# Performance work log

Measured on AMD Instinct MI355X. Metric: run time of the kernel, lower is better.

The kernel has to match this reference:

```python
import jax, jax.numpy as jnp
import numpy as np

TESS = 16            # number of tessellation cells on [0,1]
ZERO_BOUNDARY = False
N_POINTS = 16777216  # 2**24
EPS = 1e-7


def make_basis(nC, zero_boundary):
    # Constraint matrix L: continuity of v(x)=a_c x + b_c at internal vertices x_k=k/nC
    rows = []
    for k in range(1, nC):
        xk = k / nC
        r = np.zeros(2 * nC)
        r[2 * (k - 1)] = xk
        r[2 * (k - 1) + 1] = 1.0
        r[2 * k] = -xk
        r[2 * k + 1] = -1.0
        rows.append(r)
    if zero_boundary:
        r = np.zeros(2 * nC); r[1] = 1.0; rows.append(r)          # v(0)=0
        r = np.zeros(2 * nC); r[-2] = 1.0; r[-1] = 1.0; rows.append(r)  # v(1)=0
    L = np.stack(rows)
    _, _, Vh = np.linalg.svd(L, full_matrices=True)
    rank = np.linalg.matrix_rank(L)
    return np.ascontiguousarray(Vh[rank:].T).astype(np.float32)  # [2nC, d]

B_NP = make_basis(TESS, ZERO_BOUNDARY)


def setup_inputs() -> dict:
    key = jax.random.key(0)
    k1, k2 = jax.random.split(key)
    x = jax.random.uniform(k1, (N_POINTS, 1), dtype=jnp.float32)
    theta = jax.random.normal(k2, (1, B_NP.shape[1]), dtype=jnp.float32)
    return {"x": x, "theta": theta}


def cpab_integrate(grid, a, b, nC):
    """Exact closed-form integration of dx/dt = a_c x + b_c over t in [0,1].
    grid: [N]; a,b: [nC]. Returns (phi(x), log dphi/dx). At most nC cell hops."""
    h = 1.0 / nC
    c0 = jnp.clip(jnp.floor(grid * nC), 0, nC - 1).astype(jnp.int32)
    carry0 = (grid, c0, jnp.ones_like(grid), jnp.zeros_like(grid),
              jnp.zeros(grid.shape, dtype=bool))

    def step(carry, _):
        xc, c, t, phase, done = carry
        ac = a[c]
        bc = b[c]
        v = ac * xc + bc
        going_right = v >= 0
        # edge cells extend to +/- inf: moving outward never exits
        edge_out = (going_right & (c == nC - 1)) | ((~going_right) & (c == 0))
        xb = jnp.where(going_right, (c + 1).astype(grid.dtype) * h,
                       c.astype(grid.dtype) * h)
        vb = ac * xb + bc
        a_zero = jnp.abs(ac) < 1e-12
        v_zero = jnp.abs(v) < 1e-15
        ac_safe = jnp.where(a_zero, 1.0, ac)
        v_safe = jnp.where(v_zero, 1.0, v)
        ratio = vb / v_safe
        thit_lin = (xb - xc) / v_safe
        thit_aff = jnp.log(jnp.maximum(ratio, 1e-30)) / ac_safe
        thit = jnp.where(a_zero, thit_lin, thit_aff)
        reachable = (~edge_out) & (~v_zero) & (ratio > 0)
        thit = jnp.where(reachable, thit, jnp.inf)
        exit_ = (thit <= t) & (~done)
        dt = jnp.where(done, 0.0, jnp.where(exit_, thit, t))
        psi = jnp.where(a_zero, xc + v * dt,
                        (xc + bc / ac_safe) * jnp.exp(ac * dt) - bc / ac_safe)
        x_new = jnp.where(done, xc, jnp.where(exit_, xb, psi))
        phase_new = phase + jnp.where(done, 0.0, ac * dt)
        c_new = jnp.where(exit_, jnp.clip(c + jnp.where(going_right, 1, -1), 0, nC - 1), c)
        t_new = t - dt
        done_new = done | (~exit_)
        return (x_new, c_new, t_new, phase_new, done_new), None

    (xf, _, _, phase, _), _ = jax.lax.scan(step, carry0, None, length=nC)
    return xf, phase


def reference(x, theta):
    B = jnp.asarray(B_NP)
    grid = jnp.clip(x[:, 0], EPS, 1.0 - EPS)          # [N]
    A = (theta @ B.T).reshape(TESS, 2)                # theta batch of 1 -> [nC,2]
    a, b = A[:, 0], A[:, 1]
    z, phase = cpab_integrate(grid, a, b, TESS)
    # log dz/dx = sum_c a_c * dt_c = phase (log(exp(phase)) simplified)
    return z[:, None], phase[:, None]
```

## Files before the change

kernel.cpp:

```cpp
#include <hip/hip_runtime.h>
#include <math.h>

#define NCELL 16
#define BLOCK 256
#define H16 0.0625f
#define SENT 1e30f

struct BMat { float v[32][17]; };
static BMat g_B;

static struct BInitializer {
  BInitializer() {
    double A[15][32];
    for (int r = 0; r < 15; ++r)
      for (int j = 0; j < 32; ++j) A[r][j] = 0.0;
    for (int k = 1; k <= 15; ++k) {
      double xk = (double)k / 16.0;
      A[k - 1][2 * (k - 1)]     =  xk;
      A[k - 1][2 * (k - 1) + 1] =  1.0;
      A[k - 1][2 * k]           = -xk;
      A[k - 1][2 * k + 1]       = -1.0;
    }
    double V[15][32], tau[15];
    for (int i = 0; i < 15; ++i) {
      double alpha = A[i][i];
      double xn2 = 0.0;
      for (int j = i + 1; j < 32; ++j) xn2 += A[i][j] * A[i][j];
      for (int j = 0; j < 32; ++j) V[i][j] = 0.0;
      V[i][i] = 1.0;
      if (xn2 == 0.0) { tau[i] = 0.0; continue; }
      double beta = -copysign(sqrt(alpha * alpha + xn2), alpha);
      tau[i] = (beta - alpha) / beta;
      double s = 1.0 / (alpha - beta);
      for (int j = i + 1; j < 32; ++j) V[i][j] = A[i][j] * s;
      A[i][i] = beta;
      for (int r = i + 1; r < 15; ++r) {
        double dot = 0.0;
        for (int j = i; j < 32; ++j) dot += A[r][j] * V[i][j];
        double t = tau[i] * dot;
        for (int j = i; j < 32; ++j) A[r][j] -= t * V[i][j];
      }
    }
    for (int q = 0; q < 17; ++q) {
      double u[32];
      for (int p = 0; p < 32; ++p) u[p] = 0.0;
      u[15 + q] = 1.0;
      for (int i = 14; i >= 0; --i) {
        double dot = 0.0;
        for (int p = i; p < 32; ++p) dot += u[p] * V[i][p];
        double t = tau[i] * dot;
        for (int p = i; p < 32; ++p) u[p] -= t * V[i][p];
      }
      for (int p = 0; p < 32; ++p) g_B.v[p][q] = (float)u[p];
    }
  }
} g_binit;

__global__ __launch_bounds__(BLOCK) void
cpab_kernel(const float4* __restrict__ x4, const float* __restrict__ theta,
            float4* __restrict__ zout, float4* __restrict__ pout, BMat B) {
  __shared__ float Ash[32];
  __shared__ float4 cellT[2][16];
  __shared__ float vbT[2][17];
  __shared__ float lvbT[2][17];
  __shared__ float prT[2][17];

  const int tid = threadIdx.x;

  if (tid < 32) {
    float acc = 0.0f;
#pragma unroll
    for (int q = 0; q < 17; ++q) acc += theta[q] * B.v[tid][q];
    Ash[tid] = acc;
  }
  __syncthreads();

  if (tid < 32) {
    int d = tid >> 4, c = tid & 15;
    int cs = d ? 15 - c : c;
    float a = Ash[2 * cs];
    float b = d ? -(Ash[2 * cs] + Ash[2 * cs + 1]) : Ash[2 * cs + 1];
    float as = (fabsf(a) < 1e-12f) ? 1.0f : a;
    float ia = 1.0f / as;
    cellT[d][c] = make_float4(a, b, ia, b * ia);
  }
  if (tid >= 32 && tid < 66) {
    int t2 = tid - 32;
    int d = (t2 >= 17) ? 1 : 0, k = d ? t2 - 17 : t2;
    int c = min(k, 15);
    int cs = d ? 15 - c : c;
    float a = Ash[2 * cs];
    float b = d ? -(Ash[2 * cs] + Ash[2 * cs + 1]) : Ash[2 * cs + 1];
    float v = fmaf(a, (float)k * H16, b);
    vbT[d][k] = v;
    lvbT[d][k] = __logf(v);
  }
  __syncthreads();

  if (tid < 32) {
    int d = tid >> 4, c = tid & 15;
    float a = cellT[d][c].x, ia = cellT[d][c].z;
    float va = vbT[d][c], vb = vbT[d][c + 1];
    float tau;
    if (va > 0.0f && vb > 0.0f)
      tau = (fabsf(a) < 1e-12f) ? H16 / va : (lvbT[d][c + 1] - lvbT[d][c]) * ia;
    else
      tau = 2.0f;
    tau = fminf(fmaxf(tau, 0.0f), 2.0f);
    prT[d][c + 1] = tau;
  }
  __syncthreads();
  if (tid < 2) {
    float s = 0.0f;
    prT[tid][0] = 0.0f;
    for (int c = 0; c < 16; ++c) { s += prT[tid][c + 1]; prT[tid][c + 1] = s; }
  }
  __syncthreads();

  float prF[16], prM[16];
#pragma unroll
  for (int k = 0; k < 16; ++k) { prF[k] = prT[0][k]; prM[k] = prT[1][k]; }

  const int gid = blockIdx.x * BLOCK + tid;
  const float4 xs = x4[gid];
  float xin[4] = {xs.x, xs.y, xs.z, xs.w};
  float zr[4], ph[4];

#pragma unroll
  for (int p = 0; p < 4; ++p) {
    float x = fminf(fmaxf(xin[p], 1e-7f), 1.0f - 1e-7f);
    int c0 = min((int)(x * 16.0f), 15);
    float4 cf = cellT[0][c0];
    float vraw = fmaf(cf.x, x, cf.y);
    bool mir = vraw < 0.0f;
    int cw = mir ? 15 - c0 : c0;
    float xw = mir ? 1.0f - x : x;
    float a2 = cf.x;
    float ia2 = cf.z;
    float v0 = mir ? -vraw : vraw;
    bool az = fabsf(a2) < 1e-12f;
    float lv0 = __logf(v0);

    const float* vb  = vbT[mir ? 1 : 0];
    const float* lvb = lvbT[mir ? 1 : 0];
    const float* pr  = prT[mir ? 1 : 0];

    float xb = (float)(cw + 1) * H16;
    float vbn = vb[cw + 1];
    float rv = __builtin_amdgcn_rcpf(fmaxf(v0, 1e-30f));
    float t0 = az ? (xb - xw) * rv : (lvb[cw + 1] - lv0) * ia2;
    if (v0 < 1e-15f || vbn <= 0.0f) t0 = SENT;

    float prc = pr[cw + 1];
    float Tstar = 1.0f - t0 + prc;
    int m = cw;
#pragma unroll
    for (int k = 1; k <= 15; ++k) {
      float prk = mir ? prM[k] : prF[k];
      if ((k > cw) && (prk <= Tstar)) ++m;
    }
    bool moved = (m != cw);
    float4 cmv = cellT[mir ? 1 : 0][m];
    float t_enter = moved ? t0 + (pr[m] - prc) : 0.0f;
    float t_rem = 1.0f - t_enter;
    float xe = moved ? (float)m * H16 : xw;
    float ve = moved ? vb[m] : v0;
    bool az3 = fabsf(cmv.x) < 1e-12f;
    float zw = az3 ? fmaf(ve, t_rem, xe)
                   : fmaf(xe + cmv.w, __expf(cmv.x * t_rem), -cmv.w);
    zr[p] = mir ? 1.0f - zw : zw;
    ph[p] = (moved ? lvb[m] - lv0 : 0.0f) + cmv.x * t_rem;
  }

  zout[gid] = make_float4(zr[0], zr[1], zr[2], zr[3]);
  pout[gid] = make_float4(ph[0], ph[1], ph[2], ph[3]);
}

extern "C" void kernel_launch(void* const* d_in, const int* in_sizes, int n_in,
                              void* d_out, int out_size, void* d_ws, size_t ws_size,
                              hipStream_t stream) {
  const float4* x4 = (const float4*)d_in[0];
  const float* theta = (const float*)d_in[1];
  float* out = (float*)d_out;
  const int npts = in_sizes[0];
  const int groups = npts / 4;
  const int grid = groups / BLOCK;
  cpab_kernel<<<grid, BLOCK, 0, stream>>>(
      x4, theta, (float4*)out, (float4*)(out + npts), g_B);
}
```

Before: 195.5 us.

## Pack per-vertex tables into one float4 LDS array and binary-search exit cell

Merges the separate cell, boundary-velocity, log-velocity and prefix-time shared tables into a single float4 table per direction. Each lookup then needs one wide LDS read instead of several scalar ones. The 15-step linear scan over per-thread prefix arrays becomes a 4-step binary search over the shared prefix sums, which drops the 32 per-thread registers. Per-point reciprocals are now computed with rcp instead of being read from the table, which adds a little ALU work and slightly changes precision.

```diff
diff --git a/kernel.cpp b/kernel.cpp
--- a/kernel.cpp
+++ b/kernel.cpp
@@ -1,7 +1,6 @@
 #include <hip/hip_runtime.h>
 #include <math.h>
 
-#define NCELL 16
 #define BLOCK 256
 #define H16 0.0625f
 #define SENT 1e30f
@@ -60,10 +59,7 @@
 cpab_kernel(const float4* __restrict__ x4, const float* __restrict__ theta,
             float4* __restrict__ zout, float4* __restrict__ pout, BMat B) {
   __shared__ float Ash[32];
-  __shared__ float4 cellT[2][16];
-  __shared__ float vbT[2][17];
-  __shared__ float lvbT[2][17];
-  __shared__ float prT[2][17];
+  __shared__ float4 G[2][17];
 
   const int tid = threadIdx.x;
 
@@ -75,51 +71,39 @@
   }
   __syncthreads();
 
-  if (tid < 32) {
-    int d = tid >> 4, c = tid & 15;
-    int cs = d ? 15 - c : c;
-    float a = Ash[2 * cs];
-    float b = d ? -(Ash[2 * cs] + Ash[2 * cs + 1]) : Ash[2 * cs + 1];
-    float as = (fabsf(a) < 1e-12f) ? 1.0f : a;
-    float ia = 1.0f / as;
-    cellT[d][c] = make_float4(a, b, ia, b * ia);
-  }
-  if (tid >= 32 && tid < 66) {
-    int t2 = tid - 32;
-    int d = (t2 >= 17) ? 1 : 0, k = d ? t2 - 17 : t2;
-    int c = min(k, 15);
-    int cs = d ? 15 - c : c;
+  if (tid < 34) {
+    int d = (tid >= 17) ? 1 : 0, k = d ? tid - 17 : tid;
+    int c = min(k, 15), cs = d ? 15 - c : c;
     float a = Ash[2 * cs];
     float b = d ? -(Ash[2 * cs] + Ash[2 * cs + 1]) : Ash[2 * cs + 1];
     float v = fmaf(a, (float)k * H16, b);
-    vbT[d][k] = v;
-    lvbT[d][k] = __logf(v);
+    G[d][k].x = v;
+    G[d][k].y = __logf(v);
+    G[d][k].w = a;
   }
   __syncthreads();
 
   if (tid < 32) {
     int d = tid >> 4, c = tid & 15;
-    float a = cellT[d][c].x, ia = cellT[d][c].z;
-    float va = vbT[d][c], vb = vbT[d][c + 1];
+    float a = G[d][c].w;
+    float va = G[d][c].x, vb = G[d][c + 1].x;
     float tau;
-    if (va > 0.0f && vb > 0.0f)
-      tau = (fabsf(a) < 1e-12f) ? H16 / va : (lvbT[d][c + 1] - lvbT[d][c]) * ia;
-    else
+    if (va > 0.0f && vb > 0.0f) {
+      bool az = fabsf(a) < 1e-12f;
+      tau = az ? H16 / va : (G[d][c + 1].y - G[d][c].y) / a;
+    } else {
       tau = 2.0f;
+    }
     tau = fminf(fmaxf(tau, 0.0f), 2.0f);
-    prT[d][c + 1] = tau;
+    G[d][c + 1].z = tau;
   }
   __syncthreads();
   if (tid < 2) {
     float s = 0.0f;
-    prT[tid][0] = 0.0f;
-    for (int c = 0; c < 16; ++c) { s += prT[tid][c + 1]; prT[tid][c + 1] = s; }
+    G[tid][0].z = 0.0f;
+    for (int c = 1; c <= 16; ++c) { s += G[tid][c].z; G[tid][c].z = s; }
   }
   __syncthreads();
-
-  float prF[16], prM[16];
-#pragma unroll
-  for (int k = 0; k < 16; ++k) { prF[k] = prT[0][k]; prM[k] = prT[1][k]; }
 
   const int gid = blockIdx.x * BLOCK + tid;
   const float4 xs = x4[gid];
@@ -130,46 +114,47 @@
   for (int p = 0; p < 4; ++p) {
     float x = fminf(fmaxf(xin[p], 1e-7f), 1.0f - 1e-7f);
     int c0 = min((int)(x * 16.0f), 15);
-    float4 cf = cellT[0][c0];
-    float vraw = fmaf(cf.x, x, cf.y);
+    float4 g0 = G[0][c0];
+    float a = g0.w;
+    float vraw = fmaf(a, x - (float)c0 * H16, g0.x);
     bool mir = vraw < 0.0f;
     int cw = mir ? 15 - c0 : c0;
     float xw = mir ? 1.0f - x : x;
-    float a2 = cf.x;
-    float ia2 = cf.z;
     float v0 = mir ? -vraw : vraw;
-    bool az = fabsf(a2) < 1e-12f;
     float lv0 = __logf(v0);
+    bool az = fabsf(a) < 1e-12f;
+    float ia = __builtin_amdgcn_rcpf(az ? 1.0f : a);
+    const float4* Gd = G[mir ? 1 : 0];
 
-    const float* vb  = vbT[mir ? 1 : 0];
-    const float* lvb = lvbT[mir ? 1 : 0];
-    const float* pr  = prT[mir ? 1 : 0];
+    float4 gb = Gd[cw + 1];
+    float xb = (float)(cw + 1) * H16;
+    float rv = __builtin_amdgcn_rcpf(fmaxf(v0, 1e-30f));
+    float t0 = az ? (xb - xw) * rv : (gb.y - lv0) * ia;
+    if (v0 < 1e-15f || gb.x <= 0.0f) t0 = SENT;
 
-    float xb = (float)(cw + 1) * H16;
-    float vbn = vb[cw + 1];
-    float rv = __builtin_amdgcn_rcpf(fmaxf(v0, 1e-30f));
-    float t0 = az ? (xb - xw) * rv : (lvb[cw + 1] - lv0) * ia2;
-    if (v0 < 1e-15f || vbn <= 0.0f) t0 = SENT;
-
-    float prc = pr[cw + 1];
-    float Tstar = 1.0f - t0 + prc;
-    int m = cw;
+    float Tstar = 1.0f - t0 + gb.z;
+    int m = 0;
+    float prm = 0.0f;
 #pragma unroll
-    for (int k = 1; k <= 15; ++k) {
-      float prk = mir ? prM[k] : prF[k];
-      if ((k > cw) && (prk <= Tstar)) ++m;
+    for (int s = 8; s >= 1; s >>= 1) {
+      int cand = m + s;
+      float pv = Gd[cand].z;
+      if (pv <= Tstar) { m = cand; prm = pv; }
     }
-    bool moved = (m != cw);
-    float4 cmv = cellT[mir ? 1 : 0][m];
-    float t_enter = moved ? t0 + (pr[m] - prc) : 0.0f;
-    float t_rem = 1.0f - t_enter;
-    float xe = moved ? (float)m * H16 : xw;
-    float ve = moved ? vb[m] : v0;
-    bool az3 = fabsf(cmv.x) < 1e-12f;
+    bool moved = m > cw;
+    int mf = moved ? m : cw;
+    float4 gm = Gd[mf];
+    float am = gm.w;
+    bool az3 = fabsf(am) < 1e-12f;
+    float iam = __builtin_amdgcn_rcpf(az3 ? 1.0f : am);
+    float boa = fmaf(gm.x, iam, -(float)mf * H16);
+    float t_rem = moved ? (Tstar - prm) : 1.0f;
+    float xe = moved ? (float)mf * H16 : xw;
+    float ve = moved ? gm.x : v0;
     float zw = az3 ? fmaf(ve, t_rem, xe)
-                   : fmaf(xe + cmv.w, __expf(cmv.x * t_rem), -cmv.w);
+                   : fmaf(xe + boa, __expf(am * t_rem), -boa);
     zr[p] = mir ? 1.0f - zw : zw;
-    ph[p] = (moved ? lvb[m] - lv0 : 0.0f) + cmv.x * t_rem;
+    ph[p] = (moved ? gm.y - lv0 : 0.0f) + am * t_rem;
   }
 
   zout[gid] = make_float4(zr[0], zr[1], zr[2], zr[3]);
```

New measurement: 185.1 us. -5.3%, faster.
